# Performance work log

Hardware: AMD Instinct MI355X
Metric: run time of the kernel (lower is better)

Reference implementation:

```python
import jax, jax.numpy as jnp
import numpy as np

B, T, C, HS = 4, 2048, 2048, 64
H = C // HS
LW, LA, LV, LG = 64, 64, 32, 128
EPS_GN = 0.00064


def setup_inputs() -> dict:
    key = jax.random.key(0)
    ks = jax.random.split(key, 32)
    rn = lambda k, shape, s=1.0: jax.random.normal(k, shape, dtype=jnp.float32) * s
    return {
        "x": rn(ks[0], (B, T, C)),
        "v_first": rn(ks[1], (B, T, C)),
        "x_prev": rn(ks[2], (B, C)),
        "wkv_state": rn(ks[3], (B, H, HS, HS), 0.1),
        "x_r": rn(ks[4], (C,), 0.1),
        "x_w": rn(ks[5], (C,), 0.1),
        "x_k": rn(ks[6], (C,), 0.1),
        "x_v": rn(ks[7], (C,), 0.1),
        "x_a": rn(ks[8], (C,), 0.1),
        "x_g": rn(ks[9], (C,), 0.1),
        "w0": rn(ks[10], (C,), 0.1),
        "w1": rn(ks[11], (C, LW), 0.02),
        "w2": rn(ks[12], (LW, C), 0.02),
        "a0": rn(ks[13], (C,), 0.1),
        "a1": rn(ks[14], (C, LA), 0.02),
        "a2": rn(ks[15], (LA, C), 0.02),
        "v0": rn(ks[16], (C,), 0.1),
        "v1": rn(ks[17], (C, LV), 0.02),
        "v2": rn(ks[18], (LV, C), 0.02),
        "g1": rn(ks[19], (C, LG), 0.02),
        "g2": rn(ks[20], (LG, C), 0.02),
        "k_k": rn(ks[21], (C,), 0.1),
        "k_a": rn(ks[22], (C,), 0.1),
        "r_k": rn(ks[23], (H, HS), 0.1),
        "Wr": rn(ks[24], (C, C), 0.02),
        "Wk": rn(ks[25], (C, C), 0.02),
        "Wv": rn(ks[26], (C, C), 0.02),
        "Wo": rn(ks[27], (C, C), 0.02),
        "ln_w": jnp.ones((C,), dtype=jnp.float32),
        "ln_b": jnp.zeros((C,), dtype=jnp.float32),
    }


def _fwd(x, v_first, x_prev, wkv_state, x_r, x_w, x_k, x_v, x_a, x_g,
         w0, w1, w2, a0, a1, a2, v0, v1, v2, g1, g2, k_k, k_a, r_k,
         Wr, Wk, Wv, Wo, ln_w, ln_b):
    Bb, Tt, Cc = x.shape
    # token shift
    xx = jnp.concatenate([x_prev[:, None, :], x[:, :-1, :]], axis=1) - x
    xr = x + xx * x_r; xw = x + xx * x_w; xk = x + xx * x_k
    xv = x + xx * x_v; xa = x + xx * x_a; xg = x + xx * x_g
    r = xr @ Wr
    k = xk @ Wk
    v = xv @ Wv
    # log-decay: -softplus(-(w0 + tanh(xw@w1)@w2)) - 0.5  (<= -0.5)
    w_raw = -jax.nn.softplus(-(w0 + jnp.tanh(xw @ w1) @ w2)) - 0.5
    # layer_id != 0: mix with v_first
    v = v + (v_first - v) * jax.nn.sigmoid(v0 + (xv @ v1) @ v2)
    a = jax.nn.sigmoid(a0 + (xa @ a1) @ a2)
    g = jax.nn.sigmoid(xg @ g1) @ g2
    kk = (k * k_k).reshape(Bb, Tt, H, HS)
    kk = kk / jnp.maximum(jnp.linalg.norm(kk, axis=-1, keepdims=True), 1e-12)
    k = k * (1.0 + (a - 1.0) * k_a)
    rh = r.reshape(Bb, Tt, H, HS)
    kh = k.reshape(Bb, Tt, H, HS)
    vh = v.reshape(Bb, Tt, H, HS)
    ah = -kk                                  # removal direction
    bh = kk * a.reshape(Bb, Tt, H, HS)        # insertion direction
    wd = jnp.exp(-jnp.exp(w_raw)).reshape(Bb, Tt, H, HS)  # decay in (0,1)
    def step(st, ts):
        r_t, w_t, k_t, v_t, a_t, b_t = ts     # each [B,H,N]
        sa = jnp.einsum('bhij,bhj->bhi', st, a_t)
        st = st * w_t[:, :, None, :] + sa[..., None] * b_t[:, :, None, :] \
             + v_t[..., None] * k_t[:, :, None, :]
        return st, jnp.einsum('bhij,bhj->bhi', st, r_t)
    xs = tuple(jnp.moveaxis(t, 1, 0) for t in (rh, wd, kh, vh, ah, bh))
    _, out = jax.lax.scan(step, wkv_state, xs)
    out = jnp.moveaxis(out, 0, 1)             # [B,T,H,N]
    # GroupNorm(H groups) over each head's N channels
    mu = out.mean(-1, keepdims=True)
    var = out.var(-1, keepdims=True)
    out = ((out - mu) * jax.lax.rsqrt(var + EPS_GN)).reshape(Bb, Tt, Cc) * ln_w + ln_b
    bonus = (rh * kh * r_k).sum(-1, keepdims=True) * vh
    out = out + bonus.reshape(Bb, Tt, Cc)
    return (out * g) @ Wo


def reference(x, v_first, x_prev, wkv_state, x_r, x_w, x_k, x_v, x_a, x_g,
              w0, w1, w2, a0, a1, a2, v0, v1, v2, g1, g2, k_k, k_a, r_k,
              Wr, Wk, Wv, Wo, ln_w, ln_b):
    return _fwd(x, v_first, x_prev, wkv_state, x_r, x_w, x_k, x_v, x_a, x_g,
                w0, w1, w2, a0, a1, a2, v0, v1, v2, g1, g2, k_k, k_a, r_k,
                Wr, Wk, Wv, Wo, ln_w, ln_b)
```

## Files before the change

kernel.cpp:

```cpp
#include <hip/hip_runtime.h>

typedef float f32x4 __attribute__((ext_vector_type(4)));
typedef __bf16 bf16x8 __attribute__((ext_vector_type(8)));
typedef unsigned int u32x4 __attribute__((ext_vector_type(4)));

#define DI __device__ __forceinline__

constexpr int B_ = 4, T_ = 2048, C_ = 2048, H_ = 32;
constexpr int M_ = B_ * T_;

DI unsigned short f2bf(float f) {
  unsigned u = __float_as_uint(f);
  return (unsigned short)((u + 0x7FFFu + ((u >> 16) & 1u)) >> 16);
}
DI float bf2f(unsigned short h) { return __uint_as_float(((unsigned)h) << 16); }

DI void gl16(const void* g, void* l) {
  __builtin_amdgcn_global_load_lds(
      (__attribute__((address_space(1))) const unsigned int*)g,
      (__attribute__((address_space(3))) unsigned int*)l, 16, 0, 0);
}

DI float rsum8(float x) {
  int t = __builtin_amdgcn_update_dpp(0, __float_as_int(x), 0xB1, 0xF, 0xF, true);
  x += __int_as_float(t);
  t = __builtin_amdgcn_update_dpp(0, __float_as_int(x), 0x4E, 0xF, 0xF, true);
  x += __int_as_float(t);
  t = __builtin_amdgcn_update_dpp(0, __float_as_int(x), 0x141, 0xF, 0xF, true);
  x += __int_as_float(t);
  return x;
}

DI void tr_body(const float* __restrict__ in, unsigned short* __restrict__ out,
                int R, int C, int bx, int by, float (*tile)[33]) {
  int c0 = bx * 32, r0 = by * 32;
  int tx = threadIdx.x & 31, ty = threadIdx.x >> 5;
#pragma unroll
  for (int i = 0; i < 4; ++i) {
    int r = r0 + ty * 4 + i, c = c0 + tx;
    if (r < R && c < C) tile[ty * 4 + i][tx] = in[(size_t)r * C + c];
  }
  __syncthreads();
#pragma unroll
  for (int i = 0; i < 4; ++i) {
    int c = c0 + ty * 4 + i, r = r0 + tx;
    if (r < R && c < C) out[(size_t)c * R + r] = f2bf(tile[tx][ty * 4 + i]);
  }
}

__global__ __launch_bounds__(256) void k_transpose(const float* __restrict__ in,
                                                   unsigned short* __restrict__ out,
                                                   int R, int C) {
  __shared__ float tile[32][33];
  tr_body(in, out, R, C, blockIdx.x, blockIdx.y, tile);
}

__global__ __launch_bounds__(256) void k_transpose8(
    const float* w1, unsigned short* W1T, const float* a1, unsigned short* A1T,
    const float* v1, unsigned short* V1T, const float* g1, unsigned short* G1T,
    const float* w2, unsigned short* W2T, const float* a2, unsigned short* A2T,
    const float* v2, unsigned short* V2T, const float* g2, unsigned short* G2T) {
  __shared__ float tile[32][33];
  int b = blockIdx.x;
  if (b < 128)       tr_body(w1, W1T, 2048, 64, b % 2, b / 2, tile);
  else if (b < 256)  { b -= 128; tr_body(a1, A1T, 2048, 64, b % 2, b / 2, tile); }
  else if (b < 320)  { b -= 256; tr_body(v1, V1T, 2048, 32, 0, b, tile); }
  else if (b < 576)  { b -= 320; tr_body(g1, G1T, 2048, 128, b % 4, b / 4, tile); }
  else if (b < 704)  { b -= 576; tr_body(w2, W2T, 64, 2048, b % 64, b / 64, tile); }
  else if (b < 832)  { b -= 704; tr_body(a2, A2T, 64, 2048, b % 64, b / 64, tile); }
  else if (b < 896)  { b -= 832; tr_body(v2, V2T, 32, 2048, b % 64, b / 64, tile); }
  else               { b -= 896; tr_body(g2, G2T, 128, 2048, b % 64, b / 64, tile); }
}

DI void mix_emit(const float* coef, int c0, size_t off,
                 const float* xv, const float* dx, unsigned short* dst) {
  unsigned short u[8];
#pragma unroll
  for (int i = 0; i < 2; ++i) {
    f32x4 cf = *(const f32x4*)(coef + c0 + i * 4);
#pragma unroll
    for (int j = 0; j < 4; ++j) u[i * 4 + j] = f2bf(xv[i * 4 + j] + dx[i * 4 + j] * cf[j]);
  }
  u32x4 pv;
#pragma unroll
  for (int j = 0; j < 4; ++j) pv[j] = (unsigned)u[2 * j] | ((unsigned)u[2 * j + 1] << 16);
  *(u32x4*)(dst + off) = pv;
}

__global__ __launch_bounds__(256) void k_prep6(
    const float* __restrict__ x, const float* __restrict__ xprev,
    const float* __restrict__ cR, const float* __restrict__ cV,
    const float* __restrict__ cK, const float* __restrict__ cW,
    const float* __restrict__ cA, const float* __restrict__ cG,
    unsigned short* __restrict__ XR, unsigned short* __restrict__ XV,
    unsigned short* __restrict__ XK, unsigned short* __restrict__ XW,
    unsigned short* __restrict__ XA, unsigned short* __restrict__ XG) {
  int bt = blockIdx.x;
  int t = bt & (T_ - 1);
  int c0 = threadIdx.x * 8;
  size_t off = (size_t)bt * C_ + c0;
  const float* xp = x + off;
  const float* pp = t ? (xp - C_) : (xprev + (size_t)(bt >> 11) * C_ + c0);
  float xv[8], dx[8];
#pragma unroll
  for (int i = 0; i < 2; ++i) {
    f32x4 a = *(const f32x4*)(xp + i * 4);
    f32x4 p = *(const f32x4*)(pp + i * 4);
#pragma unroll
    for (int j = 0; j < 4; ++j) { xv[i * 4 + j] = a[j]; dx[i * 4 + j] = p[j] - a[j]; }
  }
  mix_emit(cR, c0, off, xv, dx, XR);
  mix_emit(cV, c0, off, xv, dx, XV);
  mix_emit(cK, c0, off, xv, dx, XK);
  mix_emit(cW, c0, off, xv, dx, XW);
  mix_emit(cA, c0, off, xv, dx, XA);
  mix_emit(cG, c0, off, xv, dx, XG);
}

template <int EPI>
__global__ __launch_bounds__(256, 2) void k_gemm_big(
    const unsigned short* __restrict__ A,
    const unsigned short* __restrict__ Bt,
    float* __restrict__ outF, unsigned short* __restrict__ outB,
    const unsigned short* __restrict__ svb, const float* __restrict__ vfirst,
    const unsigned short* __restrict__ abf,
    const float* __restrict__ k_k, const float* __restrict__ k_a,
    unsigned short* __restrict__ ahb, unsigned short* __restrict__ bhb) {
  __shared__ __align__(16) unsigned short As[128][64];
  __shared__ __align__(16) unsigned short Bs[128][64];
  const int tid = threadIdx.x, lane = tid & 63, wv = tid >> 6;
  const int bid = blockIdx.x;
  const int loc = bid >> 3;
  const int by = (bid & 7) * 8 + (loc & 7);
  const int bx = loc >> 3;
  const int m0 = by * 128, n0 = bx * 128;
  const int wm = (wv >> 1) * 64, wn = (wv & 1) * 64;
  const int lr = lane >> 3, lc = (lane & 7) * 8;
  f32x4 acc[4][4] = {};
  for (int kt = 0; kt < C_; kt += 64) {
    __syncthreads();
#pragma unroll
    for (int i = 0; i < 4; ++i) {
      int chunk = wv * 4 + i, r = chunk * 8 + lr;
      gl16(A + (size_t)(m0 + r) * C_ + kt + lc, (char*)&As[0][0] + chunk * 1024);
      gl16(Bt + (size_t)(n0 + r) * C_ + kt + lc, (char*)&Bs[0][0] + chunk * 1024);
    }
    __syncthreads();
    const int rr = lane & 15;
#pragma unroll
    for (int kh = 0; kh < 2; ++kh) {
      const int kof = kh * 32 + (lane >> 4) * 8;
      bf16x8 af[4], bfv[4];
#pragma unroll
      for (int i = 0; i < 4; ++i) af[i] = *(const bf16x8*)&As[wm + i * 16 + rr][kof];
#pragma unroll
      for (int j = 0; j < 4; ++j) bfv[j] = *(const bf16x8*)&Bs[wn + j * 16 + rr][kof];
#pragma unroll
      for (int i = 0; i < 4; ++i)
#pragma unroll
        for (int j = 0; j < 4; ++j)
          acc[i][j] = __builtin_amdgcn_mfma_f32_16x16x32_bf16(af[i], bfv[j], acc[i][j], 0, 0, 0);
    }
  }
  const int cr = (lane >> 4) * 4, cc2 = lane & 15;
  if constexpr (EPI == 2) {
    float kkv[4], kav[4];
#pragma unroll
    for (int j = 0; j < 4; ++j) {
      int col = n0 + wn + j * 16 + cc2;
      kkv[j] = k_k[col];
      kav[j] = k_a[col];
    }
#pragma unroll
    for (int i = 0; i < 4; ++i)
#pragma unroll
      for (int q = 0; q < 4; ++q) {
        int row = m0 + wm + i * 16 + cr + q;
        float kk4[4], p = 0.f;
#pragma unroll
        for (int j = 0; j < 4; ++j) {
          float kkc = acc[i][j][q] * kkv[j];
          kk4[j] = kkc;
          p += kkc * kkc;
        }
        p += __shfl_xor(p, 1); p += __shfl_xor(p, 2);
        p += __shfl_xor(p, 4); p += __shfl_xor(p, 8);
        float inv = 1.f / fmaxf(sqrtf(p), 1e-12f);
#pragma unroll
        for (int j = 0; j < 4; ++j) {
          int col = n0 + wn + j * 16 + cc2;
          size_t off = (size_t)row * C_ + col;
          float kkn = kk4[j] * inv;
          float a = bf2f(abf[off]);
          ahb[off] = f2bf(-kkn);
          bhb[off] = f2bf(kkn * a);
          outB[off] = f2bf(acc[i][j][q] * (1.f + (a - 1.f) * kav[j]));
        }
      }
  } else {
#pragma unroll
    for (int i = 0; i < 4; ++i)
#pragma unroll
      for (int j = 0; j < 4; ++j)
#pragma unroll
        for (int q = 0; q < 4; ++q) {
          int row = m0 + wm + i * 16 + cr + q;
          int col = n0 + wn + j * 16 + cc2;
          size_t off = (size_t)row * C_ + col;
          float v = acc[i][j][q];
          if constexpr (EPI == 0) {
            outB[off] = f2bf(v);
          } else if constexpr (EPI == 1) {
            float s = bf2f(svb[off]);
            outB[off] = f2bf(v + (vfirst[off] - v) * s);
          } else {
            outF[off] = v;
          }
        }
  }
}

template <int N, int ACT>
DI void down_body(int m0, unsigned short (*As)[64], unsigned short (*Bs)[64],
                  const unsigned short* __restrict__ A,
                  const unsigned short* __restrict__ Bt,
                  unsigned short* __restrict__ out) {
  const int tid = threadIdx.x, lane = tid & 63, wv = tid >> 6;
  const int wm = wv * 32;
  const int lr = lane >> 3, lc = (lane & 7) * 8;
  f32x4 acc[2][N / 16] = {};
  for (int kt = 0; kt < C_; kt += 64) {
    __syncthreads();
#pragma unroll
    for (int i = 0; i < 4; ++i) {
      int chunk = wv * 4 + i, r = chunk * 8 + lr;
      gl16(A + (size_t)(m0 + r) * C_ + kt + lc, (char*)&As[0][0] + chunk * 1024);
    }
#pragma unroll
    for (int i = 0; i < N / 32; ++i) {
      int chunk = wv * (N / 32) + i, r = chunk * 8 + lr;
      gl16(Bt + (size_t)r * C_ + kt + lc, (char*)&Bs[0][0] + chunk * 1024);
    }
    __syncthreads();
    const int rr = lane & 15;
#pragma unroll
    for (int kh = 0; kh < 2; ++kh) {
      const int kof = kh * 32 + (lane >> 4) * 8;
      bf16x8 af[2], bfv[N / 16];
#pragma unroll
      for (int i = 0; i < 2; ++i) af[i] = *(const bf16x8*)&As[wm + i * 16 + rr][kof];
#pragma unroll
      for (int j = 0; j < N / 16; ++j) bfv[j] = *(const bf16x8*)&Bs[j * 16 + rr][kof];
#pragma unroll
      for (int i = 0; i < 2; ++i)
#pragma unroll
        for (int j = 0; j < N / 16; ++j)
          acc[i][j] = __builtin_amdgcn_mfma_f32_16x16x32_bf16(af[i], bfv[j], acc[i][j], 0, 0, 0);
    }
  }
  const int cr = (lane >> 4) * 4, cc2 = lane & 15;
#pragma unroll
  for (int i = 0; i < 2; ++i)
#pragma unroll
    for (int j = 0; j < N / 16; ++j)
#pragma unroll
      for (int q = 0; q < 4; ++q) {
        int row = m0 + wm + i * 16 + cr + q;
        int col = j * 16 + cc2;
        float v = acc[i][j][q];
        if (ACT == 1) v = tanhf(v);
        else if (ACT == 2) v = 1.f / (1.f + expf(-v));
        out[(size_t)row * N + col] = f2bf(v);
      }
}

__global__ __launch_bounds__(256, 2) void k_down4(
    const unsigned short* __restrict__ XMw, const unsigned short* __restrict__ XMa,
    const unsigned short* __restrict__ XMv, const unsigned short* __restrict__ XMg,
    const unsigned short* __restrict__ W1T, const unsigned short* __restrict__ A1T,
    const unsigned short* __restrict__ V1T, const unsigned short* __restrict__ G1T,
    unsigned short* __restrict__ HWB, unsigned short* __restrict__ HAB,
    unsigned short* __restrict__ HVB, unsigned short* __restrict__ HGB) {
  __shared__ __align__(16) unsigned short As[128][64];
  __shared__ __align__(16) unsigned short Bs[128][64];
  int g = blockIdx.x >> 6;
  int m0 = (blockIdx.x & 63) * 128;
  if (g == 0)      down_body<64, 1>(m0, As, Bs, XMw, W1T, HWB);
  else if (g == 1) down_body<64, 0>(m0, As, Bs, XMa, A1T, HAB);
  else if (g == 2) down_body<32, 0>(m0, As, Bs, XMv, V1T, HVB);
  else             down_body<128, 2>(m0, As, Bs, XMg, G1T, HGB);
}

template <int K, int MODE>
__global__ __launch_bounds__(256, 2) void k_up(
    const unsigned short* __restrict__ A, const unsigned short* __restrict__ Bt,
    const float* __restrict__ bias, float* __restrict__ outF,
    unsigned short* __restrict__ outB) {
  __shared__ __align__(16) unsigned short As[128][K];
  __shared__ __align__(16) unsigned short Bs[128][K];
  const int tid = threadIdx.x, lane = tid & 63, wv = tid >> 6;
  const int m0 = blockIdx.y * 128, n0 = blockIdx.x * 128;
  const int wm = (wv >> 1) * 64, wn = (wv & 1) * 64;
  constexpr int LPR = K / 8;
  constexpr int RPC = 64 / LPR;
  const int lr = lane / LPR, lc = (lane % LPR) * 8;
  f32x4 acc[4][4] = {};
#pragma unroll
  for (int i = 0; i < K / 16; ++i) {
    int chunk = wv * (K / 16) + i;
    int r = chunk * RPC + lr;
    gl16(A + (size_t)(m0 + r) * K + lc, (char*)&As[0][0] + chunk * 1024);
    gl16(Bt + (size_t)(n0 + r) * K + lc, (char*)&Bs[0][0] + chunk * 1024);
  }
  __syncthreads();
  const int rr = lane & 15;
#pragma unroll
  for (int ks = 0; ks < K / 32; ++ks) {
    const int kof = ks * 32 + (lane >> 4) * 8;
    bf16x8 af[4], bfv[4];
#pragma unroll
    for (int i = 0; i < 4; ++i) af[i] = *(const bf16x8*)&As[wm + i * 16 + rr][kof];
#pragma unroll
    for (int j = 0; j < 4; ++j) bfv[j] = *(const bf16x8*)&Bs[wn + j * 16 + rr][kof];
#pragma unroll
    for (int i = 0; i < 4; ++i)
#pragma unroll
      for (int j = 0; j < 4; ++j)
        acc[i][j] = __builtin_amdgcn_mfma_f32_16x16x32_bf16(af[i], bfv[j], acc[i][j], 0, 0, 0);
  }
  const int cr = (lane >> 4) * 4, cc2 = lane & 15;
#pragma unroll
  for (int i = 0; i < 4; ++i)
#pragma unroll
    for (int j = 0; j < 4; ++j)
#pragma unroll
      for (int q = 0; q < 4; ++q) {
        int row = m0 + wm + i * 16 + cr + q;
        int col = n0 + wn + j * 16 + cc2;
        size_t off = (size_t)row * C_ + col;
        float up = acc[i][j][q];
        if (MODE == 0) {
          float z = -(bias[col] + up);
          float sp = fmaxf(z, 0.f) + log1pf(expf(-fabsf(z)));
          outF[off] = expf(-expf(-sp - 0.5f));
        } else if (MODE == 1) {
          outB[off] = f2bf(1.f / (1.f + expf(-(bias[col] + up))));
        } else {
          outB[off] = f2bf(up);
        }
      }
}

__global__ __launch_bounds__(64, 1) void k_scan(
    const unsigned short* __restrict__ RB, const float* __restrict__ WD,
    const unsigned short* __restrict__ KB, const unsigned short* __restrict__ VB,
    const unsigned short* __restrict__ AHB, const unsigned short* __restrict__ BHB,
    const float* __restrict__ s0, float* __restrict__ out) {
  const int lane = threadIdx.x & 63;
  const int p = blockIdx.x;
  const int wr = p >> 7, bh = p & 127;
  const int b = bh >> 5, h = bh & 31;
  const int e = lane & 7, rl = lane >> 3;
  const int row = wr * 8 + rl;
  const int e8 = e * 8;
  const size_t base = (size_t)b * T_ * C_ + h * 64;
  float S[8];
  {
    const float* sp = s0 + ((size_t)(b * H_ + h) * 64 + row) * 64 + e8;
    f32x4 s0v = *(const f32x4*)sp, s1v = *(const f32x4*)(sp + 4);
#pragma unroll
    for (int j = 0; j < 4; ++j) { S[j] = s0v[j]; S[4 + j] = s1v[j]; }
  }

#define DECL_SLOT(n) bf16x8 r##n, k##n, a##n, bb##n; f32x4 wA##n, wB##n; unsigned short v##n;
  DECL_SLOT(0) DECL_SLOT(1) DECL_SLOT(2) DECL_SLOT(3)

#define ISSUE(n, t)                                              \
  {                                                              \
    int ti = (t) < T_ ? (t) : T_ - 1;                            \
    size_t eo = base + (size_t)ti * C_;                          \
    size_t ee = eo + e8;                                         \
    r##n = *(const bf16x8*)(RB + ee);                            \
    k##n = *(const bf16x8*)(KB + ee);                            \
    a##n = *(const bf16x8*)(AHB + ee);                           \
    bb##n = *(const bf16x8*)(BHB + ee);                          \
    wA##n = *(const f32x4*)(WD + ee);                            \
    wB##n = *(const f32x4*)(WD + ee + 4);                        \
    v##n = VB[eo + row];                                         \
  }

#define STEP(n, t)                                               \
  {                                                              \
    float rr[8], kk[8], aa[8], bv[8], ww[8];                     \
    _Pragma("unroll") for (int j = 0; j < 8; ++j) {              \
      rr[j] = (float)r##n[j];                                    \
      kk[j] = (float)k##n[j];                                    \
      aa[j] = (float)a##n[j];                                    \
      bv[j] = (float)bb##n[j];                                   \
    }                                                            \
    _Pragma("unroll") for (int j = 0; j < 4; ++j) {              \
      ww[j] = wA##n[j];                                          \
      ww[4 + j] = wB##n[j];                                      \
    }                                                            \
    float sa0 = S[0] * aa[0], sa1 = S[1] * aa[1];                \
    _Pragma("unroll") for (int j = 2; j < 8; j += 2) {           \
      sa0 = fmaf(S[j], aa[j], sa0);                              \
      sa1 = fmaf(S[j + 1], aa[j + 1], sa1);                      \
    }                                                            \
    float sa = rsum8(sa0 + sa1);                                 \
    float vi = bf2f(v##n);                                       \
    float o0 = 0.f, o1 = 0.f;                                    \
    _Pragma("unroll") for (int j = 0; j < 8; j += 2) {           \
      S[j] = fmaf(S[j], ww[j], fmaf(sa, bv[j], vi * kk[j]));     \
      S[j + 1] = fmaf(S[j + 1], ww[j + 1],                       \
                      fmaf(sa, bv[j + 1], vi * kk[j + 1]));      \
      o0 = fmaf(S[j], rr[j], o0);                                \
      o1 = fmaf(S[j + 1], rr[j + 1], o1);                        \
    }                                                            \
    float o = rsum8(o0 + o1);                                    \
    if (e == 0) out[base + (size_t)(t) * C_ + row] = o;          \
  }

  ISSUE(0, 0) ISSUE(1, 1) ISSUE(2, 2)
#pragma unroll 1
  for (int t = 0; t < T_; t += 4) {
    ISSUE(3, t + 3) STEP(0, t)
    ISSUE(0, t + 4) STEP(1, t + 1)
    ISSUE(1, t + 5) STEP(2, t + 2)
    ISSUE(2, t + 6) STEP(3, t + 3)
  }
#undef DECL_SLOT
#undef ISSUE
#undef STEP
}

__global__ __launch_bounds__(256) void k_gn(
    const float* __restrict__ o, const unsigned short* __restrict__ rb,
    const unsigned short* __restrict__ kb, const unsigned short* __restrict__ v,
    const unsigned short* __restrict__ g, const float* __restrict__ r_k,
    const float* __restrict__ lnw, const float* __restrict__ lnb,
    unsigned short* __restrict__ outg) {
  int wid = blockIdx.x * 4 + (threadIdx.x >> 6);
  int lane = threadIdx.x & 63;
  int h = wid & (H_ - 1);
  size_t bt = (size_t)(wid >> 5);
  size_t off = bt * C_ + h * 64 + lane;
  int c = h * 64 + lane;
  float x = o[off];
  float mu = x;
#pragma unroll
  for (int m = 1; m < 64; m <<= 1) mu += __shfl_xor(mu, m);
  mu *= (1.f / 64.f);
  float d = x - mu;
  float var = d * d;
#pragma unroll
  for (int m = 1; m < 64; m <<= 1) var += __shfl_xor(var, m);
  var *= (1.f / 64.f);
  float y = d * rsqrtf(var + 6.4e-4f) * lnw[c] + lnb[c];
  float bd = bf2f(rb[off]) * bf2f(kb[off]) * r_k[c];
#pragma unroll
  for (int m = 1; m < 64; m <<= 1) bd += __shfl_xor(bd, m);
  float res = (y + bd * bf2f(v[off])) * bf2f(g[off]);
  outg[off] = f2bf(res);
}

extern "C" void kernel_launch(void* const* d_in, const int* in_sizes, int n_in,
                              void* d_out, int out_size, void* d_ws, size_t ws_size,
                              hipStream_t stream) {
  const float* x      = (const float*)d_in[0];
  const float* vfirst = (const float*)d_in[1];
  const float* xprev  = (const float*)d_in[2];
  const float* wkv0   = (const float*)d_in[3];
  const float* x_r = (const float*)d_in[4];
  const float* x_w = (const float*)d_in[5];
  const float* x_k = (const float*)d_in[6];
  const float* x_v = (const float*)d_in[7];
  const float* x_a = (const float*)d_in[8];
  const float* x_g = (const float*)d_in[9];
  const float* w0 = (const float*)d_in[10];
  const float* w1 = (const float*)d_in[11];
  const float* w2 = (const float*)d_in[12];
  const float* a0 = (const float*)d_in[13];
  const float* a1 = (const float*)d_in[14];
  const float* a2 = (const float*)d_in[15];
  const float* v0 = (const float*)d_in[16];
  const float* v1 = (const float*)d_in[17];
  const float* v2 = (const float*)d_in[18];
  const float* g1 = (const float*)d_in[19];
  const float* g2 = (const float*)d_in[20];
  const float* k_k = (const float*)d_in[21];
  const float* k_a = (const float*)d_in[22];
  const float* r_k = (const float*)d_in[23];
  const float* Wr = (const float*)d_in[24];
  const float* Wk = (const float*)d_in[25];
  const float* Wv = (const float*)d_in[26];
  const float* Wo = (const float*)d_in[27];
  const float* lnw = (const float*)d_in[28];
  const float* lnb = (const float*)d_in[29];
  float* out = (float*)d_out;
  char* ws = (char*)d_ws;

  size_t woff = 0;
  auto alloc = [&](size_t n) { char* p = ws + woff; woff += n; return p; };
  char* R1 = alloc(67108864);
  unsigned short* ABF = (unsigned short*)R1;
  unsigned short* SVB = (unsigned short*)(R1 + 33554432);
  float* WD = (float*)R1;
  unsigned short* WT  = (unsigned short*)alloc(8388608);
  unsigned short* W1T = (unsigned short*)alloc(262144);
  unsigned short* A1T = (unsigned short*)alloc(262144);
  unsigned short* V1T = (unsigned short*)alloc(131072);
  unsigned short* G1T = (unsigned short*)alloc(524288);
  unsigned short* W2T = (unsigned short*)alloc(262144);
  unsigned short* A2T = (unsigned short*)alloc(262144);
  unsigned short* V2T = (unsigned short*)alloc(131072);
  unsigned short* G2T = (unsigned short*)alloc(524288);
  unsigned short* HWB = (unsigned short*)alloc(1048576);
  unsigned short* HAB = (unsigned short*)alloc(1048576);
  unsigned short* HVB = (unsigned short*)alloc(524288);
  unsigned short* HGB = (unsigned short*)alloc(2097152);
  unsigned short* RB  = (unsigned short*)alloc(33554432);
  unsigned short* KB  = (unsigned short*)alloc(33554432);
  unsigned short* VB  = (unsigned short*)alloc(33554432);
  unsigned short* AHB = (unsigned short*)alloc(33554432);
  unsigned short* BHB = (unsigned short*)alloc(33554432);
  alloc(65536);
  unsigned short* XMr = VB;
  unsigned short* XMv = KB;
  unsigned short* XMk = (unsigned short*)out;
  unsigned short* XMw = AHB;
  unsigned short* XMa = BHB;
  unsigned short* XMg = RB;
  unsigned short* GBF  = AHB;
  unsigned short* OUTG = BHB;

  dim3 blk(256);
  dim3 gg(16, 64);
  dim3 g1d(1024);

  k_transpose8<<<dim3(1152), blk, 0, stream>>>(w1, W1T, a1, A1T, v1, V1T, g1, G1T,
                                               w2, W2T, a2, A2T, v2, V2T, g2, G2T);

  k_prep6<<<dim3(M_), blk, 0, stream>>>(x, xprev, x_r, x_v, x_k, x_w, x_a, x_g,
                                        XMr, XMv, XMk, XMw, XMa, XMg);

  k_down4<<<dim3(256), blk, 0, stream>>>(XMw, XMa, XMv, XMg,
                                         W1T, A1T, V1T, G1T, HWB, HAB, HVB, HGB);

  k_up<64, 1><<<gg, blk, 0, stream>>>(HAB, A2T, a0, nullptr, ABF);
  k_up<32, 1><<<gg, blk, 0, stream>>>(HVB, V2T, v0, nullptr, SVB);

  k_transpose<<<dim3(64, 64), blk, 0, stream>>>(Wr, WT, 2048, 2048);
  k_gemm_big<0><<<g1d, blk, 0, stream>>>(XMr, WT,
      nullptr, RB, nullptr, nullptr, nullptr, nullptr, nullptr, nullptr, nullptr);

  k_transpose<<<dim3(64, 64), blk, 0, stream>>>(Wv, WT, 2048, 2048);
  k_gemm_big<1><<<g1d, blk, 0, stream>>>(XMv, WT,
      nullptr, VB, SVB, vfirst, nullptr, nullptr, nullptr, nullptr, nullptr);

  k_transpose<<<dim3(64, 64), blk, 0, stream>>>(Wk, WT, 2048, 2048);
  k_gemm_big<2><<<g1d, blk, 0, stream>>>(XMk, WT,
      nullptr, KB, nullptr, nullptr, ABF, k_k, k_a, AHB, BHB);

  k_up<64, 0><<<gg, blk, 0, stream>>>(HWB, W2T, w0, WD, nullptr);

  k_scan<<<dim3(1024), dim3(64), 0, stream>>>(RB, WD, KB, VB, AHB, BHB, wkv0, out);

  k_up<128, 3><<<gg, blk, 0, stream>>>(HGB, G2T, nullptr, nullptr, GBF);

  k_gn<<<dim3(65536), blk, 0, stream>>>(out, RB, KB, VB, GBF, r_k, lnw, lnb, OUTG);

  k_transpose<<<dim3(64, 64), blk, 0, stream>>>(Wo, WT, 2048, 2048);
  k_gemm_big<3><<<g1d, blk, 0, stream>>>(OUTG, WT,
      out, nullptr, nullptr, nullptr, nullptr, nullptr, nullptr, nullptr, nullptr);
}
```

Baseline: 1.361 ms.

## Stage scan inputs through LDS with async global-to-LDS loads and deeper prefetch

The recurrent scan kernel now loads each timestep's r/k/a/b/w/v head slices into an 8-slot LDS ring buffer with global_load_lds, and issues them four steps ahead. Register fetches are replaced by LDS reads. The per-lane loads are coalesced 4-byte copies, so each wave fetches only what the head needs once instead of duplicating loads per lane. The kernel waits on vmcnt manually, and the launch bound no longer forces one block per SIMD, which may allow more occupancy. The risks are added LDS latency and correctness of the hand-written waitcnt and the missing barrier.

```diff
diff --git a/kernel.cpp b/kernel.cpp
--- a/kernel.cpp
+++ b/kernel.cpp
@@ -19,6 +19,11 @@
   __builtin_amdgcn_global_load_lds(
       (__attribute__((address_space(1))) const unsigned int*)g,
       (__attribute__((address_space(3))) unsigned int*)l, 16, 0, 0);
+}
+DI void gl4(const void* g, void* l) {
+  __builtin_amdgcn_global_load_lds(
+      (__attribute__((address_space(1))) const unsigned int*)g,
+      (__attribute__((address_space(3))) unsigned int*)l, 4, 0, 0);
 }
 
 DI float rsum8(float x) {
@@ -351,85 +356,96 @@
       }
 }
 
-__global__ __launch_bounds__(64, 1) void k_scan(
+__global__ __launch_bounds__(64) void k_scan(
     const unsigned short* __restrict__ RB, const float* __restrict__ WD,
     const unsigned short* __restrict__ KB, const unsigned short* __restrict__ VB,
     const unsigned short* __restrict__ AHB, const unsigned short* __restrict__ BHB,
     const float* __restrict__ s0, float* __restrict__ out) {
+  __shared__ __align__(16) char sl[8][1024];
   const int lane = threadIdx.x & 63;
   const int p = blockIdx.x;
   const int wr = p >> 7, bh = p & 127;
   const int b = bh >> 5, h = bh & 31;
   const int e = lane & 7, rl = lane >> 3;
   const int row = wr * 8 + rl;
-  const int e8 = e * 8;
+  const int e16 = e * 16;
   const size_t base = (size_t)b * T_ * C_ + h * 64;
   float S[8];
   {
-    const float* sp = s0 + ((size_t)(b * H_ + h) * 64 + row) * 64 + e8;
+    const float* sp = s0 + ((size_t)(b * H_ + h) * 64 + row) * 64 + e * 8;
     f32x4 s0v = *(const f32x4*)sp, s1v = *(const f32x4*)(sp + 4);
 #pragma unroll
     for (int j = 0; j < 4; ++j) { S[j] = s0v[j]; S[4 + j] = s1v[j]; }
   }
 
-#define DECL_SLOT(n) bf16x8 r##n, k##n, a##n, bb##n; f32x4 wA##n, wB##n; unsigned short v##n;
-  DECL_SLOT(0) DECL_SLOT(1) DECL_SLOT(2) DECL_SLOT(3)
-
-#define ISSUE(n, t)                                              \
-  {                                                              \
-    int ti = (t) < T_ ? (t) : T_ - 1;                            \
-    size_t eo = base + (size_t)ti * C_;                          \
-    size_t ee = eo + e8;                                         \
-    r##n = *(const bf16x8*)(RB + ee);                            \
-    k##n = *(const bf16x8*)(KB + ee);                            \
-    a##n = *(const bf16x8*)(AHB + ee);                           \
-    bb##n = *(const bf16x8*)(BHB + ee);                          \
-    wA##n = *(const f32x4*)(WD + ee);                            \
-    wB##n = *(const f32x4*)(WD + ee + 4);                        \
-    v##n = VB[eo + row];                                         \
-  }
-
-#define STEP(n, t)                                               \
-  {                                                              \
-    float rr[8], kk[8], aa[8], bv[8], ww[8];                     \
-    _Pragma("unroll") for (int j = 0; j < 8; ++j) {              \
-      rr[j] = (float)r##n[j];                                    \
-      kk[j] = (float)k##n[j];                                    \
-      aa[j] = (float)a##n[j];                                    \
-      bv[j] = (float)bb##n[j];                                   \
-    }                                                            \
-    _Pragma("unroll") for (int j = 0; j < 4; ++j) {              \
-      ww[j] = wA##n[j];                                          \
-      ww[4 + j] = wB##n[j];                                      \
-    }                                                            \
-    float sa0 = S[0] * aa[0], sa1 = S[1] * aa[1];                \
-    _Pragma("unroll") for (int j = 2; j < 8; j += 2) {           \
-      sa0 = fmaf(S[j], aa[j], sa0);                              \
-      sa1 = fmaf(S[j + 1], aa[j + 1], sa1);                      \
-    }                                                            \
-    float sa = rsum8(sa0 + sa1);                                 \
-    float vi = bf2f(v##n);                                       \
-    float o0 = 0.f, o1 = 0.f;                                    \
-    _Pragma("unroll") for (int j = 0; j < 8; j += 2) {           \
-      S[j] = fmaf(S[j], ww[j], fmaf(sa, bv[j], vi * kk[j]));     \
-      S[j + 1] = fmaf(S[j + 1], ww[j + 1],                       \
-                      fmaf(sa, bv[j + 1], vi * kk[j + 1]));      \
-      o0 = fmaf(S[j], rr[j], o0);                                \
-      o1 = fmaf(S[j + 1], rr[j + 1], o1);                        \
-    }                                                            \
-    float o = rsum8(o0 + o1);                                    \
-    if (e == 0) out[base + (size_t)(t) * C_ + row] = o;          \
-  }
-
-  ISSUE(0, 0) ISSUE(1, 1) ISSUE(2, 2)
+#define ISSUE(t, slot)                                                        \
+  {                                                                           \
+    int ti = (t) < T_ ? (t) : T_ - 1;                                         \
+    size_t eo = base + (size_t)ti * C_;                                       \
+    char* d = &sl[slot][0];                                                   \
+    const char* s1 = lane < 32 ? (const char*)(RB + eo) + lane * 4            \
+                               : (const char*)(KB + eo) + (lane - 32) * 4;    \
+    gl4(s1, d);                                                               \
+    const char* s2 = lane < 32 ? (const char*)(AHB + eo) + lane * 4           \
+                               : (const char*)(BHB + eo) + (lane - 32) * 4;   \
+    gl4(s2, d + 256);                                                         \
+    gl4((const char*)(WD + eo) + lane * 4, d + 512);                          \
+    gl4((const char*)(VB + eo) + lane * 4, d + 768);                          \
+  }
+
+#define STEP(t, slot)                                                         \
+  {                                                                           \
+    asm volatile("s_waitcnt vmcnt(16)" ::: "memory");                         \
+    __builtin_amdgcn_sched_barrier(0);                                        \
+    const char* bp = &sl[slot][0];                                            \
+    bf16x8 rv8 = *(const bf16x8*)(bp + e16);                                  \
+    bf16x8 kv8 = *(const bf16x8*)(bp + 128 + e16);                            \
+    bf16x8 av8 = *(const bf16x8*)(bp + 256 + e16);                            \
+    bf16x8 bv8 = *(const bf16x8*)(bp + 384 + e16);                            \
+    f32x4 w0 = *(const f32x4*)(bp + 512 + e * 32);                            \
+    f32x4 w1 = *(const f32x4*)(bp + 528 + e * 32);                            \
+    float vi = bf2f(*(const unsigned short*)(bp + 768 + row * 2));            \
+    float rr[8], kk[8], aa[8], bv[8], ww[8];                                  \
+    _Pragma("unroll") for (int j = 0; j < 8; ++j) {                           \
+      rr[j] = (float)rv8[j];                                                  \
+      kk[j] = (float)kv8[j];                                                  \
+      aa[j] = (float)av8[j];                                                  \
+      bv[j] = (float)bv8[j];                                                  \
+    }                                                                         \
+    _Pragma("unroll") for (int j = 0; j < 4; ++j) {                           \
+      ww[j] = w0[j];                                                          \
+      ww[4 + j] = w1[j];                                                      \
+    }                                                                         \
+    float sa0 = S[0] * aa[0], sa1 = S[1] * aa[1];                             \
+    _Pragma("unroll") for (int j = 2; j < 8; j += 2) {                        \
+      sa0 = fmaf(S[j], aa[j], sa0);                                           \
+      sa1 = fmaf(S[j + 1], aa[j + 1], sa1);                                   \
+    }                                                                         \
+    float sa = rsum8(sa0 + sa1);                                              \
+    float o0 = 0.f, o1 = 0.f;                                                 \
+    _Pragma("unroll") for (int j = 0; j < 8; j += 2) {                        \
+      S[j] = fmaf(S[j], ww[j], fmaf(sa, bv[j], vi * kk[j]));                  \
+      S[j + 1] = fmaf(S[j + 1], ww[j + 1],                                    \
+                      fmaf(sa, bv[j + 1], vi * kk[j + 1]));                   \
+      o0 = fmaf(S[j], rr[j], o0);                                             \
+      o1 = fmaf(S[j + 1], rr[j + 1], o1);                                     \
+    }                                                                         \
+    float o = rsum8(o0 + o1);                                                 \
+    if (e == 0) out[base + (size_t)(t) * C_ + row] = o;                       \
+  }
+
+  ISSUE(0, 0) ISSUE(1, 1) ISSUE(2, 2) ISSUE(3, 3)
 #pragma unroll 1
-  for (int t = 0; t < T_; t += 4) {
-    ISSUE(3, t + 3) STEP(0, t)
-    ISSUE(0, t + 4) STEP(1, t + 1)
-    ISSUE(1, t + 5) STEP(2, t + 2)
-    ISSUE(2, t + 6) STEP(3, t + 3)
-  }
-#undef DECL_SLOT
+  for (int t = 0; t < T_; t += 8) {
+    ISSUE(t + 4, 4)  STEP(t + 0, 0)
+    ISSUE(t + 5, 5)  STEP(t + 1, 1)
+    ISSUE(t + 6, 6)  STEP(t + 2, 2)
+    ISSUE(t + 7, 7)  STEP(t + 3, 3)
+    ISSUE(t + 8, 0)  STEP(t + 4, 4)
+    ISSUE(t + 9, 1)  STEP(t + 5, 5)
+    ISSUE(t + 10, 2) STEP(t + 6, 6)
+    ISSUE(t + 11, 3) STEP(t + 7, 7)
+  }
 #undef ISSUE
 #undef STEP
 }
```

Result: slower. 1.458 ms (+7.1%).
